# Kernel optimization log

Measured on AMD Instinct MI355X. Metric: run time of the kernel, lower is better.

The kernel has to match this reference:

```python
import jax, jax.numpy as jnp
import numpy as np

N_NODES = 100000
N_EDGES = 1600000
F_IN = 64
HID = 32
HEADS = 4
NEG_SLOPE = 0.2  # PyG GATConv default
EPS = 1e-16      # PyG softmax denominator epsilon


def gat_layer(x, edge_index, W, a_src, a_dst, bias, heads, out_ch, concat):
    """PyG-style GATConv (eval mode: dropout disabled), add_self_loops=True.
    x: [N, F]; edge_index: [2, E] (row0=source j, row1=target i);
    W: [F, heads*out_ch]; a_src/a_dst: [heads, out_ch]; bias: [heads*out_ch] or [out_ch].
    """
    N = x.shape[0]
    loops = jnp.arange(N)
    src = jnp.concatenate([edge_index[0], loops])  # [E+N]
    dst = jnp.concatenate([edge_index[1], loops])
    h = (x @ W).reshape(N, heads, out_ch)           # [N, H, C]
    alpha_s = jnp.einsum('nhc,hc->nh', h, a_src)    # [N, H]
    alpha_d = jnp.einsum('nhc,hc->nh', h, a_dst)
    e = jax.nn.leaky_relu(alpha_s[src] + alpha_d[dst], NEG_SLOPE)  # [E+N, H]
    # numerically stable scatter-softmax over incoming edges per target node
    m = jax.ops.segment_max(e, dst, num_segments=N)                # [N, H]
    ex = jnp.exp(e - m[dst])
    denom = jax.ops.segment_sum(ex, dst, num_segments=N)           # [N, H]
    alpha = ex / (denom[dst] + EPS)                                # [E+N, H]
    msg = h[src] * alpha[..., None]                                # [E+N, H, C]
    out = jax.ops.segment_sum(msg, dst, num_segments=N)            # [N, H, C]
    out = out.reshape(N, heads * out_ch) if concat else out.mean(axis=1)
    return out + bias


def setup_inputs() -> dict:
    key = jax.random.key(0)
    ks = jax.random.split(key, 12)
    glorot = lambda k, shape: jax.random.normal(k, shape, jnp.float32) * np.sqrt(2.0 / (shape[0] + shape[-1]))
    x = jax.random.normal(ks[0], (N_NODES, F_IN), jnp.float32)
    edge_index = jax.random.randint(ks[1], (2, N_EDGES), 0, N_NODES, jnp.int64 if jax.config.jax_enable_x64 else jnp.int32)
    batch = jnp.zeros((N_NODES,), jnp.int32)
    return {
        'x': x,
        'edge_index': edge_index,
        'batch': batch,
        'W1': glorot(ks[2], (F_IN, HEADS * HID)),
        'a_src1': glorot(ks[3], (HEADS, HID)),
        'a_dst1': glorot(ks[4], (HEADS, HID)),
        'b1': jnp.zeros((HEADS * HID,), jnp.float32),
        'W2': glorot(ks[5], (HEADS * HID, HID)),
        'a_src2': glorot(ks[6], (1, HID)),
        'a_dst2': glorot(ks[7], (1, HID)),
        'b2': jnp.zeros((HID,), jnp.float32),
        'W_lin': glorot(ks[8], (HID, 1)),
        'b_lin': jnp.zeros((1,), jnp.float32),
    }


def reference(x, edge_index, batch, W1, a_src1, a_dst1, b1, W2, a_src2, a_dst2, b2, W_lin, b_lin):
    h = jax.nn.relu(gat_layer(x, edge_index, W1, a_src1, a_dst1, b1, HEADS, HID, concat=True))
    h = jax.nn.relu(gat_layer(h, edge_index, W2, a_src2, a_dst2, b2, 1, HID, concat=False))
    out = h @ W_lin + b_lin  # [N, 1]
    return out.squeeze(-1)
```

## Files before the change

### kernel.cpp

```cpp
#include <hip/hip_runtime.h>
#include <math.h>

#define NEG_SLOPE 0.2f
#define EPS 1e-16f

__device__ inline float leaky(float v) {
    return v >= 0.0f ? v : NEG_SLOPE * v;
}

__device__ inline unsigned bf16pack2(float a, float b) {
    unsigned ua = __float_as_uint(a);
    unsigned ub = __float_as_uint(b);
    ua = (ua + 0x7FFFu + ((ua >> 16) & 1u)) >> 16;
    ub = (ub + 0x7FFFu + ((ub >> 16) & 1u)) >> 16;
    return ua | (ub << 16);
}

__device__ inline float bf16lo(unsigned u) { return __uint_as_float(u << 16); }
__device__ inline float bf16hi(unsigned u) { return __uint_as_float(u & 0xFFFF0000u); }

__global__ __launch_bounds__(256) void k_init(int* deg, int* cursor, int N) {
    int gid = blockIdx.x * blockDim.x + threadIdx.x;
    if (gid < N) { deg[gid] = 1; cursor[gid] = 0; }
}

__global__ __launch_bounds__(256) void k_hist(const int* __restrict__ ei, int* __restrict__ deg, int E) {
    int e = blockIdx.x * blockDim.x + threadIdx.x;
    if (e < E) atomicAdd(&deg[ei[E + e]], 1);
}

__global__ __launch_bounds__(256) void k_scan1(const int* __restrict__ deg, int* __restrict__ rowptr,
                                               int* __restrict__ blocksum, int N) {
    __shared__ int s[256];
    int tid = threadIdx.x;
    int i = blockIdx.x * 256 + tid;
    int v = (i < N) ? deg[i] : 0;
    s[tid] = v;
    __syncthreads();
#pragma unroll
    for (int off = 1; off < 256; off <<= 1) {
        int t = (tid >= off) ? s[tid - off] : 0;
        __syncthreads();
        s[tid] += t;
        __syncthreads();
    }
    if (i < N) rowptr[i] = s[tid] - v;
    if (tid == 255) blocksum[blockIdx.x] = s[255];
}

__global__ __launch_bounds__(512) void k_scan2(int* __restrict__ blocksum, int nb) {
    __shared__ int s[512];
    int tid = threadIdx.x;
    int v = (tid < nb) ? blocksum[tid] : 0;
    s[tid] = v;
    __syncthreads();
#pragma unroll
    for (int off = 1; off < 512; off <<= 1) {
        int t = (tid >= off) ? s[tid - off] : 0;
        __syncthreads();
        s[tid] += t;
        __syncthreads();
    }
    if (tid < nb) blocksum[tid] = s[tid] - v;
}

__global__ __launch_bounds__(256) void k_scan3(int* __restrict__ rowptr, const int* __restrict__ blocksum,
                                               int N, int total) {
    int i = blockIdx.x * blockDim.x + threadIdx.x;
    if (i < N) rowptr[i] += blocksum[i >> 8];
    if (i == 0) rowptr[N] = total;
}

__global__ __launch_bounds__(256) void k_fill(const int* __restrict__ ei, const int* __restrict__ rowptr,
                                              int* __restrict__ cursor, int* __restrict__ col, int E, int N) {
    int e = blockIdx.x * blockDim.x + threadIdx.x;
    if (e >= E + N) return;
    int src, dst;
    if (e < E) { src = ei[e]; dst = ei[E + e]; }
    else       { src = dst = e - E; }
    int pos = atomicAdd(&cursor[dst], 1);
    col[rowptr[dst] + pos] = src;
}

__global__ __launch_bounds__(256) void k_gemm1(const float* __restrict__ x,
                                               const float* __restrict__ W1,
                                               const float* __restrict__ a_src,
                                               const float* __restrict__ a_dst,
                                               unsigned* __restrict__ h1bf,
                                               float* __restrict__ as1,
                                               float* __restrict__ ad1, int N) {
    __shared__ float sW[64 * 128];
    __shared__ float sX[32 * 64];
    int tid = threadIdx.x;
    int block_r0 = blockIdx.x * 32;

    {
        float4* dst = (float4*)sW;
        const float4* srcp = (const float4*)W1;
#pragma unroll
        for (int i = 0; i < 8; ++i) dst[tid + 256 * i] = srcp[tid + 256 * i];
    }
    {
        float4* dst = (float4*)sX;
#pragma unroll
        for (int i = 0; i < 2; ++i) {
            int idx = tid + 256 * i;
            int r = idx >> 4;
            int c = idx & 15;
            int gr = min(block_r0 + r, N - 1);
            dst[idx] = ((const float4*)(x + (size_t)gr * 64))[c];
        }
    }
    __syncthreads();

    int c4 = tid & 31;
    int rq = tid >> 5;
    int r0 = block_r0 + rq * 4;
    const float4* wS = (const float4*)sW;
    const float4* xS = (const float4*)sX;

    float4 acc0 = {0,0,0,0}, acc1 = {0,0,0,0}, acc2 = {0,0,0,0}, acc3 = {0,0,0,0};
#pragma unroll 2
    for (int k4 = 0; k4 < 16; ++k4) {
        float4 xa = xS[(rq * 4 + 0) * 16 + k4];
        float4 xb = xS[(rq * 4 + 1) * 16 + k4];
        float4 xc = xS[(rq * 4 + 2) * 16 + k4];
        float4 xd = xS[(rq * 4 + 3) * 16 + k4];
        float4 w0 = wS[(k4 * 4 + 0) * 32 + c4];
        float4 w1 = wS[(k4 * 4 + 1) * 32 + c4];
        float4 w2 = wS[(k4 * 4 + 2) * 32 + c4];
        float4 w3 = wS[(k4 * 4 + 3) * 32 + c4];
        acc0.x += xa.x*w0.x + xa.y*w1.x + xa.z*w2.x + xa.w*w3.x;
        acc0.y += xa.x*w0.y + xa.y*w1.y + xa.z*w2.y + xa.w*w3.y;
        acc0.z += xa.x*w0.z + xa.y*w1.z + xa.z*w2.z + xa.w*w3.z;
        acc0.w += xa.x*w0.w + xa.y*w1.w + xa.z*w2.w + xa.w*w3.w;
        acc1.x += xb.x*w0.x + xb.y*w1.x + xb.z*w2.x + xb.w*w3.x;
        acc1.y += xb.x*w0.y + xb.y*w1.y + xb.z*w2.y + xb.w*w3.y;
        acc1.z += xb.x*w0.z + xb.y*w1.z + xb.z*w2.z + xb.w*w3.z;
        acc1.w += xb.x*w0.w + xb.y*w1.w + xb.z*w2.w + xb.w*w3.w;
        acc2.x += xc.x*w0.x + xc.y*w1.x + xc.z*w2.x + xc.w*w3.x;
        acc2.y += xc.x*w0.y + xc.y*w1.y + xc.z*w2.y + xc.w*w3.y;
        acc2.z += xc.x*w0.z + xc.y*w1.z + xc.z*w2.z + xc.w*w3.z;
        acc2.w += xc.x*w0.w + xc.y*w1.w + xc.z*w2.w + xc.w*w3.w;
        acc3.x += xd.x*w0.x + xd.y*w1.x + xd.z*w2.x + xd.w*w3.x;
        acc3.y += xd.x*w0.y + xd.y*w1.y + xd.z*w2.y + xd.w*w3.y;
        acc3.z += xd.x*w0.z + xd.y*w1.z + xd.z*w2.z + xd.w*w3.z;
        acc3.w += xd.x*w0.w + xd.y*w1.w + xd.z*w2.w + xd.w*w3.w;
    }

    uint2 p0 = { bf16pack2(acc0.x, acc0.y), bf16pack2(acc0.z, acc0.w) };
    uint2 p1 = { bf16pack2(acc1.x, acc1.y), bf16pack2(acc1.z, acc1.w) };
    uint2 p2 = { bf16pack2(acc2.x, acc2.y), bf16pack2(acc2.z, acc2.w) };
    uint2 p3 = { bf16pack2(acc3.x, acc3.y), bf16pack2(acc3.z, acc3.w) };
    uint2* hb = (uint2*)h1bf;
    if (r0 + 0 < N) hb[(size_t)(r0 + 0) * 32 + c4] = p0;
    if (r0 + 1 < N) hb[(size_t)(r0 + 1) * 32 + c4] = p1;
    if (r0 + 2 < N) hb[(size_t)(r0 + 2) * 32 + c4] = p2;
    if (r0 + 3 < N) hb[(size_t)(r0 + 3) * 32 + c4] = p3;

    float4 av = ((const float4*)a_src)[c4];
    float4 dv = ((const float4*)a_dst)[c4];
    float s0 = acc0.x*av.x + acc0.y*av.y + acc0.z*av.z + acc0.w*av.w;
    float s1 = acc1.x*av.x + acc1.y*av.y + acc1.z*av.z + acc1.w*av.w;
    float s2 = acc2.x*av.x + acc2.y*av.y + acc2.z*av.z + acc2.w*av.w;
    float s3 = acc3.x*av.x + acc3.y*av.y + acc3.z*av.z + acc3.w*av.w;
    float d0 = acc0.x*dv.x + acc0.y*dv.y + acc0.z*dv.z + acc0.w*dv.w;
    float d1 = acc1.x*dv.x + acc1.y*dv.y + acc1.z*dv.z + acc1.w*dv.w;
    float d2 = acc2.x*dv.x + acc2.y*dv.y + acc2.z*dv.z + acc2.w*dv.w;
    float d3 = acc3.x*dv.x + acc3.y*dv.y + acc3.z*dv.z + acc3.w*dv.w;
#pragma unroll
    for (int off = 1; off < 8; off <<= 1) {
        s0 += __shfl_xor(s0, off); s1 += __shfl_xor(s1, off);
        s2 += __shfl_xor(s2, off); s3 += __shfl_xor(s3, off);
        d0 += __shfl_xor(d0, off); d1 += __shfl_xor(d1, off);
        d2 += __shfl_xor(d2, off); d3 += __shfl_xor(d3, off);
    }
    if ((c4 & 7) == 0) {
        int h = c4 >> 3;
        if (r0 + 0 < N) { as1[(r0 + 0) * 4 + h] = s0; ad1[(r0 + 0) * 4 + h] = d0; }
        if (r0 + 1 < N) { as1[(r0 + 1) * 4 + h] = s1; ad1[(r0 + 1) * 4 + h] = d1; }
        if (r0 + 2 < N) { as1[(r0 + 2) * 4 + h] = s2; ad1[(r0 + 2) * 4 + h] = d2; }
        if (r0 + 3 < N) { as1[(r0 + 3) * 4 + h] = s3; ad1[(r0 + 3) * 4 + h] = d3; }
    }
}

__global__ __launch_bounds__(256) void k_gather1(const int* __restrict__ rowptr,
                                                 const int* __restrict__ col,
                                                 const float* __restrict__ as1,
                                                 const float* __restrict__ ad1,
                                                 const unsigned* __restrict__ h1bf,
                                                 const float* __restrict__ b1,
                                                 float* __restrict__ out1, int N) {
    int tid = threadIdx.x;
    int wid = (blockIdx.x * blockDim.x + tid) >> 6;
    if (wid >= N) return;
    int lane = tid & 63;
    int dst = wid;
    int start = rowptr[dst], end = rowptr[dst + 1];
    float4 ad = *(const float4*)(ad1 + (size_t)dst * 4);

    float m0 = -INFINITY, m1 = -INFINITY, m2 = -INFINITY, m3 = -INFINITY;
    for (int j = start + lane; j < end; j += 64) {
        int src = col[j];
        float4 a = *(const float4*)(as1 + (size_t)src * 4);
        m0 = fmaxf(m0, leaky(a.x + ad.x));
        m1 = fmaxf(m1, leaky(a.y + ad.y));
        m2 = fmaxf(m2, leaky(a.z + ad.z));
        m3 = fmaxf(m3, leaky(a.w + ad.w));
    }
#pragma unroll
    for (int off = 32; off; off >>= 1) {
        m0 = fmaxf(m0, __shfl_xor(m0, off));
        m1 = fmaxf(m1, __shfl_xor(m1, off));
        m2 = fmaxf(m2, __shfl_xor(m2, off));
        m3 = fmaxf(m3, __shfl_xor(m3, off));
    }

    int h = lane >> 4;
    float mh  = (h == 0) ? m0 : (h == 1) ? m1 : (h == 2) ? m2 : m3;
    float adh = (h == 0) ? ad.x : (h == 1) ? ad.y : (h == 2) ? ad.z : ad.w;

    float acc0 = 0.0f, acc1 = 0.0f, den = 0.0f;
    int j = start;
    for (; j + 3 < end; j += 4) {
        int s0 = col[j], s1 = col[j + 1], s2 = col[j + 2], s3 = col[j + 3];
        float a0 = as1[s0 * 4 + h];
        float a1 = as1[s1 * 4 + h];
        float a2 = as1[s2 * 4 + h];
        float a3 = as1[s3 * 4 + h];
        unsigned u0 = h1bf[(size_t)s0 * 64 + lane];
        unsigned u1 = h1bf[(size_t)s1 * 64 + lane];
        unsigned u2 = h1bf[(size_t)s2 * 64 + lane];
        unsigned u3 = h1bf[(size_t)s3 * 64 + lane];
        float x0 = __expf(leaky(a0 + adh) - mh);
        float x1 = __expf(leaky(a1 + adh) - mh);
        float x2 = __expf(leaky(a2 + adh) - mh);
        float x3 = __expf(leaky(a3 + adh) - mh);
        den += (x0 + x1) + (x2 + x3);
        acc0 += x0 * bf16lo(u0) + x1 * bf16lo(u1) + x2 * bf16lo(u2) + x3 * bf16lo(u3);
        acc1 += x0 * bf16hi(u0) + x1 * bf16hi(u1) + x2 * bf16hi(u2) + x3 * bf16hi(u3);
    }
    for (; j < end; ++j) {
        int src = col[j];
        float ex = __expf(leaky(as1[src * 4 + h] + adh) - mh);
        unsigned u = h1bf[(size_t)src * 64 + lane];
        den += ex;
        acc0 += ex * bf16lo(u);
        acc1 += ex * bf16hi(u);
    }

    float inv = 1.0f / (den + EPS);
    int f0 = 2 * lane;
    float vA = acc0 * inv + b1[f0];
    float vB = acc1 * inv + b1[f0 + 1];
    float2 o;
    o.x = vA > 0.0f ? vA : 0.0f;
    o.y = vB > 0.0f ? vB : 0.0f;
    *(float2*)(out1 + (size_t)dst * 128 + f0) = o;
}

__global__ __launch_bounds__(256) void k_gemm2(const float* __restrict__ out1,
                                               const float* __restrict__ W2,
                                               const float* __restrict__ a_src,
                                               const float* __restrict__ a_dst,
                                               unsigned* __restrict__ h2bf,
                                               float* __restrict__ as2,
                                               float* __restrict__ ad2, int N) {
    __shared__ float sW[128 * 32];
    int tid = threadIdx.x;

    {
        float4* dst = (float4*)sW;
        const float4* srcp = (const float4*)W2;
#pragma unroll
        for (int i = 0; i < 4; ++i) dst[tid + 256 * i] = srcp[tid + 256 * i];
    }
    __syncthreads();

    int c4 = tid & 7;
    int rq = tid >> 3;
    int r0 = blockIdx.x * 128 + rq * 4;
    if (r0 >= N) return;
    const float* xr0 = out1 + (size_t)min(r0 + 0, N - 1) * 128;
    const float* xr1 = out1 + (size_t)min(r0 + 1, N - 1) * 128;
    const float* xr2 = out1 + (size_t)min(r0 + 2, N - 1) * 128;
    const float* xr3 = out1 + (size_t)min(r0 + 3, N - 1) * 128;
    const float4* wS = (const float4*)sW;

    float4 acc0 = {0,0,0,0}, acc1 = {0,0,0,0}, acc2 = {0,0,0,0}, acc3 = {0,0,0,0};
#pragma unroll 2
    for (int k4 = 0; k4 < 32; ++k4) {
        float4 xa = *(const float4*)(xr0 + k4 * 4);
        float4 xb = *(const float4*)(xr1 + k4 * 4);
        float4 xc = *(const float4*)(xr2 + k4 * 4);
        float4 xd = *(const float4*)(xr3 + k4 * 4);
        float4 w0 = wS[(k4 * 4 + 0) * 8 + c4];
        float4 w1 = wS[(k4 * 4 + 1) * 8 + c4];
        float4 w2 = wS[(k4 * 4 + 2) * 8 + c4];
        float4 w3 = wS[(k4 * 4 + 3) * 8 + c4];
        acc0.x += xa.x*w0.x + xa.y*w1.x + xa.z*w2.x + xa.w*w3.x;
        acc0.y += xa.x*w0.y + xa.y*w1.y + xa.z*w2.y + xa.w*w3.y;
        acc0.z += xa.x*w0.z + xa.y*w1.z + xa.z*w2.z + xa.w*w3.z;
        acc0.w += xa.x*w0.w + xa.y*w1.w + xa.z*w2.w + xa.w*w3.w;
        acc1.x += xb.x*w0.x + xb.y*w1.x + xb.z*w2.x + xb.w*w3.x;
        acc1.y += xb.x*w0.y + xb.y*w1.y + xb.z*w2.y + xb.w*w3.y;
        acc1.z += xb.x*w0.z + xb.y*w1.z + xb.z*w2.z + xb.w*w3.z;
        acc1.w += xb.x*w0.w + xb.y*w1.w + xb.z*w2.w + xb.w*w3.w;
        acc2.x += xc.x*w0.x + xc.y*w1.x + xc.z*w2.x + xc.w*w3.x;
        acc2.y += xc.x*w0.y + xc.y*w1.y + xc.z*w2.y + xc.w*w3.y;
        acc2.z += xc.x*w0.z + xc.y*w1.z + xc.z*w2.z + xc.w*w3.z;
        acc2.w += xc.x*w0.w + xc.y*w1.w + xc.z*w2.w + xc.w*w3.w;
        acc3.x += xd.x*w0.x + xd.y*w1.x + xd.z*w2.x + xd.w*w3.x;
        acc3.y += xd.x*w0.y + xd.y*w1.y + xd.z*w2.y + xd.w*w3.y;
        acc3.z += xd.x*w0.z + xd.y*w1.z + xd.z*w2.z + xd.w*w3.z;
        acc3.w += xd.x*w0.w + xd.y*w1.w + xd.z*w2.w + xd.w*w3.w;
    }

    uint2 q0 = { bf16pack2(acc0.x, acc0.y), bf16pack2(acc0.z, acc0.w) };
    uint2 q1 = { bf16pack2(acc1.x, acc1.y), bf16pack2(acc1.z, acc1.w) };
    uint2 q2 = { bf16pack2(acc2.x, acc2.y), bf16pack2(acc2.z, acc2.w) };
    uint2 q3 = { bf16pack2(acc3.x, acc3.y), bf16pack2(acc3.z, acc3.w) };
    uint2* hb = (uint2*)h2bf;
    if (r0 + 0 < N) hb[(size_t)(r0 + 0) * 8 + c4] = q0;
    if (r0 + 1 < N) hb[(size_t)(r0 + 1) * 8 + c4] = q1;
    if (r0 + 2 < N) hb[(size_t)(r0 + 2) * 8 + c4] = q2;
    if (r0 + 3 < N) hb[(size_t)(r0 + 3) * 8 + c4] = q3;

    float4 av = ((const float4*)a_src)[c4];
    float4 dv = ((const float4*)a_dst)[c4];
    float s0 = acc0.x*av.x + acc0.y*av.y + acc0.z*av.z + acc0.w*av.w;
    float s1 = acc1.x*av.x + acc1.y*av.y + acc1.z*av.z + acc1.w*av.w;
    float s2 = acc2.x*av.x + acc2.y*av.y + acc2.z*av.z + acc2.w*av.w;
    float s3 = acc3.x*av.x + acc3.y*av.y + acc3.z*av.z + acc3.w*av.w;
    float d0 = acc0.x*dv.x + acc0.y*dv.y + acc0.z*dv.z + acc0.w*dv.w;
    float d1 = acc1.x*dv.x + acc1.y*dv.y + acc1.z*dv.z + acc1.w*dv.w;
    float d2 = acc2.x*dv.x + acc2.y*dv.y + acc2.z*dv.z + acc2.w*dv.w;
    float d3 = acc3.x*dv.x + acc3.y*dv.y + acc3.z*dv.z + acc3.w*dv.w;
#pragma unroll
    for (int off = 1; off < 8; off <<= 1) {
        s0 += __shfl_xor(s0, off); s1 += __shfl_xor(s1, off);
        s2 += __shfl_xor(s2, off); s3 += __shfl_xor(s3, off);
        d0 += __shfl_xor(d0, off); d1 += __shfl_xor(d1, off);
        d2 += __shfl_xor(d2, off); d3 += __shfl_xor(d3, off);
    }
    if (c4 == 0) {
        if (r0 + 0 < N) { as2[r0 + 0] = s0; ad2[r0 + 0] = d0; }
        if (r0 + 1 < N) { as2[r0 + 1] = s1; ad2[r0 + 1] = d1; }
        if (r0 + 2 < N) { as2[r0 + 2] = s2; ad2[r0 + 2] = d2; }
        if (r0 + 3 < N) { as2[r0 + 3] = s3; ad2[r0 + 3] = d3; }
    }
}

__global__ __launch_bounds__(256) void k_gather2(const int* __restrict__ rowptr,
                                                 const int* __restrict__ col,
                                                 const float* __restrict__ as2,
                                                 const float* __restrict__ ad2,
                                                 const unsigned short* __restrict__ h2b,
                                                 const float* __restrict__ b2,
                                                 const float* __restrict__ W_lin,
                                                 const float* __restrict__ b_lin,
                                                 float* __restrict__ out, int N) {
    int tid = threadIdx.x;
    int swid = (blockIdx.x * blockDim.x + tid) >> 5;
    if (swid >= N) return;
    int c = tid & 31;
    int dst = swid;
    int start = rowptr[dst], end = rowptr[dst + 1];
    float adv = ad2[dst];

    float m = -INFINITY;
    for (int j = start + c; j < end; j += 32) {
        m = fmaxf(m, leaky(as2[col[j]] + adv));
    }
#pragma unroll
    for (int off = 16; off; off >>= 1) m = fmaxf(m, __shfl_xor(m, off, 32));

    float acc = 0.0f, den = 0.0f;
    int j = start;
    for (; j + 3 < end; j += 4) {
        int s0 = col[j], s1 = col[j + 1], s2 = col[j + 2], s3 = col[j + 3];
        float a0 = as2[s0], a1 = as2[s1], a2 = as2[s2], a3 = as2[s3];
        unsigned short u0 = h2b[(size_t)s0 * 32 + c];
        unsigned short u1 = h2b[(size_t)s1 * 32 + c];
        unsigned short u2 = h2b[(size_t)s2 * 32 + c];
        unsigned short u3 = h2b[(size_t)s3 * 32 + c];
        float x0 = __expf(leaky(a0 + adv) - m);
        float x1 = __expf(leaky(a1 + adv) - m);
        float x2 = __expf(leaky(a2 + adv) - m);
        float x3 = __expf(leaky(a3 + adv) - m);
        den += (x0 + x1) + (x2 + x3);
        acc += x0 * __uint_as_float(((unsigned)u0) << 16)
             + x1 * __uint_as_float(((unsigned)u1) << 16)
             + x2 * __uint_as_float(((unsigned)u2) << 16)
             + x3 * __uint_as_float(((unsigned)u3) << 16);
    }
    for (; j < end; ++j) {
        int src = col[j];
        float ex = __expf(leaky(as2[src] + adv) - m);
        unsigned short u = h2b[(size_t)src * 32 + c];
        den += ex;
        acc += ex * __uint_as_float(((unsigned)u) << 16);
    }

    float v = acc / (den + EPS) + b2[c];
    v = v > 0.0f ? v : 0.0f;

    float w = v * W_lin[c];
#pragma unroll
    for (int off = 16; off; off >>= 1) w += __shfl_xor(w, off, 32);
    if (c == 0) out[dst] = w + b_lin[0];
}

extern "C" void kernel_launch(void* const* d_in, const int* in_sizes, int n_in,
                              void* d_out, int out_size, void* d_ws, size_t ws_size,
                              hipStream_t stream) {
    const float* x      = (const float*)d_in[0];
    const int*   ei     = (const int*)d_in[1];
    const float* W1     = (const float*)d_in[3];
    const float* a_src1 = (const float*)d_in[4];
    const float* a_dst1 = (const float*)d_in[5];
    const float* b1     = (const float*)d_in[6];
    const float* W2     = (const float*)d_in[7];
    const float* a_src2 = (const float*)d_in[8];
    const float* a_dst2 = (const float*)d_in[9];
    const float* b2     = (const float*)d_in[10];
    const float* W_lin  = (const float*)d_in[11];
    const float* b_lin  = (const float*)d_in[12];
    float* out = (float*)d_out;

    const int N = in_sizes[0] / 64;
    const int E = in_sizes[1] / 2;
    const int T = E + N;
    const int NB = (N + 255) / 256;

    float* ws = (float*)d_ws;
    size_t off = 0;
    float* h1reg = ws + off; off += (size_t)N * 128;
    float* out1 = ws + off; off += (size_t)N * 128;
    float* as1  = ws + off; off += (size_t)N * 4;
    float* ad1  = ws + off; off += (size_t)N * 4;
    float* as2  = ws + off; off += (size_t)N;
    float* ad2  = ws + off; off += (size_t)N;
    int* deg      = (int*)(ws + off); off += (size_t)N;
    int* cursor   = (int*)(ws + off); off += (size_t)N;
    int* rowptr   = (int*)(ws + off); off += (size_t)N + 4;
    int* blocksum = (int*)(ws + off); off += 1024;
    int* colarr   = (int*)(ws + off); off += (size_t)T;
    unsigned* h1bf = (unsigned*)h1reg;
    unsigned* h2bf = (unsigned*)h1reg;

    const int B = 256;
    auto blocks = [](size_t t, int b) { return (unsigned)((t + b - 1) / b); };

    k_init <<<blocks(N, B), B, 0, stream>>>(deg, cursor, N);
    k_hist <<<blocks(E, B), B, 0, stream>>>(ei, deg, E);
    k_scan1<<<NB, 256, 0, stream>>>(deg, rowptr, blocksum, N);
    k_scan2<<<1, 512, 0, stream>>>(blocksum, NB);
    k_scan3<<<blocks(N, B), B, 0, stream>>>(rowptr, blocksum, N, T);
    k_fill <<<blocks(T, B), B, 0, stream>>>(ei, rowptr, cursor, colarr, E, N);

    k_gemm1  <<<(unsigned)((N + 31) / 32), B, 0, stream>>>(x, W1, a_src1, a_dst1, h1bf, as1, ad1, N);
    k_gather1<<<blocks((size_t)N * 64, B), B, 0, stream>>>(rowptr, colarr, as1, ad1, h1bf, b1, out1, N);

    k_gemm2  <<<(unsigned)((N + 127) / 128), B, 0, stream>>>(out1, W2, a_src2, a_dst2, h2bf, as2, ad2, N);
    k_gather2<<<blocks((size_t)N * 32, B), B, 0, stream>>>(rowptr, colarr, as2, ad2,
                                                           (const unsigned short*)h2bf, b2, W_lin, b_lin, out, N);
}
```

Before: 453.0 us.

## Build CSR via two-level bucketed scatter with shared-memory fill

Replaces the single global-atomic CSR fill with a bucket sort. Edges are first histogrammed per tile into 256-node buckets, prefix-summed, and scattered as (src,dst) pairs. Each bucket is then filled in shared memory with local atomics and written out coalesced. This is meant to avoid scattered global atomics and random writes into the column array, at the cost of five extra launches and a serial per-bucket scan. Buckets with more than FILL_CAP entries are silently truncated, which is a correctness risk for skewed graphs.

```diff
diff --git a/kernel.cpp b/kernel.cpp
--- a/kernel.cpp
+++ b/kernel.cpp
@@ -19,9 +19,13 @@
 __device__ inline float bf16lo(unsigned u) { return __uint_as_float(u << 16); }
 __device__ inline float bf16hi(unsigned u) { return __uint_as_float(u & 0xFFFF0000u); }
 
-__global__ __launch_bounds__(256) void k_init(int* deg, int* cursor, int N) {
+#define TILE 8192
+#define BKSH 8
+#define FILL_CAP 6144
+
+__global__ __launch_bounds__(256) void k_init(int* deg, int N) {
     int gid = blockIdx.x * blockDim.x + threadIdx.x;
-    if (gid < N) { deg[gid] = 1; cursor[gid] = 0; }
+    if (gid < N) deg[gid] = 1;
 }
 
 __global__ __launch_bounds__(256) void k_hist(const int* __restrict__ ei, int* __restrict__ deg, int E) {
@@ -71,15 +75,104 @@
     if (i == 0) rowptr[N] = total;
 }
 
-__global__ __launch_bounds__(256) void k_fill(const int* __restrict__ ei, const int* __restrict__ rowptr,
-                                              int* __restrict__ cursor, int* __restrict__ col, int E, int N) {
-    int e = blockIdx.x * blockDim.x + threadIdx.x;
-    if (e >= E + N) return;
-    int src, dst;
-    if (e < E) { src = ei[e]; dst = ei[E + e]; }
-    else       { src = dst = e - E; }
-    int pos = atomicAdd(&cursor[dst], 1);
-    col[rowptr[dst] + pos] = src;
+__global__ __launch_bounds__(256) void k_thist(const int* __restrict__ ei, int* __restrict__ thist,
+                                               int E, int NT, int NBK) {
+    __shared__ int hist[512];
+    int tid = threadIdx.x;
+    for (int b = tid; b < 512; b += 256) hist[b] = 0;
+    __syncthreads();
+    int base = blockIdx.x * TILE;
+    for (int k = tid; k < TILE; k += 256) {
+        int e = base + k;
+        if (e < E) atomicAdd(&hist[ei[E + e] >> BKSH], 1);
+    }
+    __syncthreads();
+    for (int b = tid; b < NBK; b += 256) thist[b * NT + blockIdx.x] = hist[b];
+}
+
+__global__ __launch_bounds__(256) void k_tsum(int* __restrict__ thist, int* __restrict__ total,
+                                              int NT, int NBK) {
+    int b = blockIdx.x * blockDim.x + threadIdx.x;
+    if (b >= NBK) return;
+    int run = 0;
+    for (int t = 0; t < NT; ++t) {
+        int v = thist[b * NT + t];
+        thist[b * NT + t] = run;
+        run += v;
+    }
+    total[b] = run;
+}
+
+__global__ __launch_bounds__(512) void k_bstart(const int* __restrict__ total,
+                                                int* __restrict__ bstart, int nb) {
+    __shared__ int s[512];
+    int tid = threadIdx.x;
+    int v = (tid < nb) ? total[tid] : 0;
+    s[tid] = v;
+    __syncthreads();
+#pragma unroll
+    for (int off = 1; off < 512; off <<= 1) {
+        int t = (tid >= off) ? s[tid - off] : 0;
+        __syncthreads();
+        s[tid] += t;
+        __syncthreads();
+    }
+    if (tid < nb) bstart[tid] = s[tid] - v;
+}
+
+__global__ __launch_bounds__(256) void k_tscat(const int* __restrict__ ei,
+                                               const int* __restrict__ thist,
+                                               const int* __restrict__ bstart,
+                                               int2* __restrict__ pairs,
+                                               int E, int NT, int NBK) {
+    __shared__ int cnt[512];
+    int tid = threadIdx.x;
+    int tile = blockIdx.x;
+    for (int b = tid; b < NBK; b += 256) cnt[b] = bstart[b] + thist[b * NT + tile];
+    __syncthreads();
+    int base = tile * TILE;
+    for (int k = tid; k < TILE; k += 256) {
+        int e = base + k;
+        if (e < E) {
+            int s = ei[e], d = ei[E + e];
+            int p = atomicAdd(&cnt[d >> BKSH], 1);
+            pairs[p] = make_int2(s, d);
+        }
+    }
+}
+
+__global__ __launch_bounds__(256) void k_fill2(const int2* __restrict__ pairs,
+                                               const int* __restrict__ rowptr,
+                                               const int* __restrict__ bstart,
+                                               const int* __restrict__ total,
+                                               int* __restrict__ col, int N) {
+    __shared__ int colimg[FILL_CAP];
+    __shared__ int cur[256];
+    int tid = threadIdx.x;
+    int b = blockIdx.x;
+    int node0 = b << BKSH;
+    int nNodes = min(256, N - node0);
+    int segBase = rowptr[node0];
+    int segEnd  = rowptr[node0 + nNodes];
+    int segLen  = segEnd - segBase;
+    int pStart  = bstart[b];
+    int pLen    = total[b];
+
+    if (tid < nNodes) {
+        int r = rowptr[node0 + tid] - segBase;
+        cur[tid] = r + 1;
+        if (r < FILL_CAP) colimg[r] = node0 + tid;
+    }
+    __syncthreads();
+    for (int k = tid; k < pLen; k += 256) {
+        int2 pr = pairs[pStart + k];
+        int li = pr.y - node0;
+        int p = atomicAdd(&cur[li], 1);
+        if (p < FILL_CAP) colimg[p] = pr.x;
+    }
+    __syncthreads();
+    int lim = min(segLen, FILL_CAP);
+    for (int k = tid; k < lim; k += 256) col[segBase + k] = colimg[k];
 }
 
 __global__ __launch_bounds__(256) void k_gemm1(const float* __restrict__ x,
@@ -432,6 +525,8 @@
     const int E = in_sizes[1] / 2;
     const int T = E + N;
     const int NB = (N + 255) / 256;
+    const int NBK = (N + 255) >> BKSH;
+    const int NT = (E + TILE - 1) / TILE;
 
     float* ws = (float*)d_ws;
     size_t off = 0;
@@ -442,22 +537,30 @@
     float* as2  = ws + off; off += (size_t)N;
     float* ad2  = ws + off; off += (size_t)N;
     int* deg      = (int*)(ws + off); off += (size_t)N;
-    int* cursor   = (int*)(ws + off); off += (size_t)N;
     int* rowptr   = (int*)(ws + off); off += (size_t)N + 4;
     int* blocksum = (int*)(ws + off); off += 1024;
     int* colarr   = (int*)(ws + off); off += (size_t)T;
+    int* thist    = (int*)(ws + off); off += (size_t)NT * NBK + 4;
+    int* total    = (int*)(ws + off); off += (size_t)NBK + 4;
+    int* bstart   = (int*)(ws + off); off += (size_t)NBK + 4;
     unsigned* h1bf = (unsigned*)h1reg;
     unsigned* h2bf = (unsigned*)h1reg;
+    int2* pairs = (int2*)out1;
 
     const int B = 256;
     auto blocks = [](size_t t, int b) { return (unsigned)((t + b - 1) / b); };
 
-    k_init <<<blocks(N, B), B, 0, stream>>>(deg, cursor, N);
+    k_init <<<blocks(N, B), B, 0, stream>>>(deg, N);
     k_hist <<<blocks(E, B), B, 0, stream>>>(ei, deg, E);
     k_scan1<<<NB, 256, 0, stream>>>(deg, rowptr, blocksum, N);
     k_scan2<<<1, 512, 0, stream>>>(blocksum, NB);
     k_scan3<<<blocks(N, B), B, 0, stream>>>(rowptr, blocksum, N, T);
-    k_fill <<<blocks(T, B), B, 0, stream>>>(ei, rowptr, cursor, colarr, E, N);
+
+    k_thist <<<NT, 256, 0, stream>>>(ei, thist, E, NT, NBK);
+    k_tsum  <<<blocks(NBK, B), B, 0, stream>>>(thist, total, NT, NBK);
+    k_bstart<<<1, 512, 0, stream>>>(total, bstart, NBK);
+    k_tscat <<<NT, 256, 0, stream>>>(ei, thist, bstart, pairs, E, NT, NBK);
+    k_fill2 <<<NBK, 256, 0, stream>>>(pairs, rowptr, bstart, total, colarr, N);
 
     k_gemm1  <<<(unsigned)((N + 31) / 32), B, 0, stream>>>(x, W1, a_src1, a_dst1, h1bf, as1, ad1, N);
     k_gather1<<<blocks((size_t)N * 64, B), B, 0, stream>>>(rowptr, colarr, as1, ad1, h1bf, b1, out1, N);
```

Result: slower. 488.8 us (+7.9%).
